# Optimization experiments

Hardware: AMD Instinct MI355X
Metric: run time of the kernel (lower is better)

## Reference

```python
import jax, jax.numpy as jnp
import numpy as np

N_NODES = 50000
N_EDGES = 640000
IN, HID, OUT = 128, 128, 64


def _sage_layer(x, src, dst, w_self, w_neigh, b):
    # DGL SAGEConv 'mean': fc_self(x) + fc_neigh(mean_{u in N(v)} x_u) + bias
    n = x.shape[0]
    deg = jax.ops.segment_sum(jnp.ones_like(src, dtype=x.dtype), dst, num_segments=n)
    neigh_sum = jax.ops.segment_sum(x[src], dst, num_segments=n)  # [N, F] irregular gather+reduce
    neigh = neigh_sum / jnp.maximum(deg, 1.0)[:, None]
    return x @ w_self + neigh @ w_neigh + b


def setup_inputs() -> dict:
    key = jax.random.key(0)
    ks = jax.random.split(key, 16)
    s = lambda fan_in: 1.0 / np.sqrt(fan_in)
    return {
        "x": jax.random.normal(ks[0], (N_NODES, IN), dtype=jnp.float32),
        "src": jax.random.randint(ks[1], (N_EDGES,), 0, N_NODES, dtype=jnp.int32),
        "dst": jax.random.randint(ks[2], (N_EDGES,), 0, N_NODES, dtype=jnp.int32),
        "w_self1": jax.random.normal(ks[3], (IN, HID), dtype=jnp.float32) * s(IN),
        "w_neigh1": jax.random.normal(ks[4], (IN, HID), dtype=jnp.float32) * s(IN),
        "b1": jnp.zeros((HID,), dtype=jnp.float32),
        "w_self2": jax.random.normal(ks[5], (HID, HID), dtype=jnp.float32) * s(HID),
        "w_neigh2": jax.random.normal(ks[6], (HID, HID), dtype=jnp.float32) * s(HID),
        "b2": jnp.zeros((HID,), dtype=jnp.float32),
        "w_self3": jax.random.normal(ks[7], (HID, OUT), dtype=jnp.float32) * s(HID),
        "w_neigh3": jax.random.normal(ks[8], (HID, OUT), dtype=jnp.float32) * s(HID),
        "b3": jnp.zeros((OUT,), dtype=jnp.float32),
    }


def reference(x, src, dst, w_self1, w_neigh1, b1, w_self2, w_neigh2, b2, w_self3, w_neigh3, b3):
    h = _sage_layer(x, src, dst, w_self1, w_neigh1, b1)
    h = jax.nn.relu(h)  # dropout omitted (eval mode)
    h = _sage_layer(h, src, dst, w_self2, w_neigh2, b2)
    h = jax.nn.relu(h)
    h = _sage_layer(h, src, dst, w_self3, w_neigh3, b3)
    return h
```

## Files before the change

kernel.cpp:

```cpp
#include <hip/hip_runtime.h>

static constexpr int F = 128;
static constexpr int MAXB = 32;

typedef __attribute__((ext_vector_type(8))) short bf16x8;
typedef __attribute__((ext_vector_type(4))) float f32x4;
typedef __attribute__((ext_vector_type(2))) float f32x2;

__device__ __forceinline__ unsigned short f2b(float f) {
    unsigned int u = __float_as_uint(f);
    u += 0x7fffu + ((u >> 16) & 1u);
    return (unsigned short)(u >> 16);
}
__device__ __forceinline__ float b2f(unsigned int s) {
    return __uint_as_float(s << 16);
}

#if __has_builtin(__builtin_elementwise_fma)
__device__ __forceinline__ f32x2 fma2(f32x2 a, f32x2 b, f32x2 c) { return __builtin_elementwise_fma(a, b, c); }
#else
__device__ __forceinline__ f32x2 fma2(f32x2 a, f32x2 b, f32x2 c) {
    f32x2 r; r[0] = fmaf(a[0], b[0], c[0]); r[1] = fmaf(a[1], b[1], c[1]); return r;
}
#endif

#if __has_builtin(__builtin_amdgcn_cvt_pk_f32_fp8) && __has_builtin(__builtin_amdgcn_cvt_pk_fp8_f32)
__device__ __forceinline__ f32x2 q2f_lo(unsigned int d) { return __builtin_amdgcn_cvt_pk_f32_fp8(d, false); }
__device__ __forceinline__ f32x2 q2f_hi(unsigned int d) { return __builtin_amdgcn_cvt_pk_f32_fp8(d, true);  }
__device__ __forceinline__ unsigned int f2q_pk4(float a, float b, float c, float d) {
    int p = __builtin_amdgcn_cvt_pk_fp8_f32(a, b, 0, false);
    p = __builtin_amdgcn_cvt_pk_fp8_f32(c, d, p, true);
    return (unsigned int)p;
}
__device__ __forceinline__ unsigned char f2q1(float v) {
    return (unsigned char)(__builtin_amdgcn_cvt_pk_fp8_f32(v, v, 0, false) & 0xff);
}
#else
__device__ __forceinline__ float q2f1(unsigned int b) {
    const unsigned s = b >> 7, e = (b >> 3) & 15, m = b & 7;
    float v = e ? __uint_as_float(((e - 7 + 127) << 23) | (m << 20))
                : (float)m * 0.001953125f;
    return s ? -v : v;
}
__device__ __forceinline__ f32x2 q2f_lo(unsigned int d) { f32x2 r; r[0] = q2f1(d & 0xff); r[1] = q2f1((d >> 8) & 0xff); return r; }
__device__ __forceinline__ f32x2 q2f_hi(unsigned int d) { f32x2 r; r[0] = q2f1((d >> 16) & 0xff); r[1] = q2f1((d >> 24) & 0xff); return r; }
__device__ __forceinline__ unsigned char f2q1(float f) {
    float cf = fminf(fmaxf(f, -448.f), 448.f);
    unsigned u = __float_as_uint(cf);
    unsigned s = (u >> 31) << 7;
    int e = (int)((u >> 23) & 255) - 127;
    unsigned m = u & 0x7fffff;
    if (e < -6) return (unsigned char)s;
    unsigned keep = m >> 20, rest = m & 0xfffff;
    keep += (rest > 0x80000u) || (rest == 0x80000u && (keep & 1));
    e += (int)(keep >> 3); keep &= 7;
    if (e > 8) { e = 8; keep = 6; }
    return (unsigned char)(s | ((unsigned)(e + 7) << 3) | keep);
}
__device__ __forceinline__ unsigned int f2q_pk4(float a, float b, float c, float d) {
    return (unsigned)f2q1(a) | ((unsigned)f2q1(b) << 8) | ((unsigned)f2q1(c) << 16) | ((unsigned)f2q1(d) << 24);
}
#endif

__global__ __launch_bounds__(256) void prep_kernel(const float* __restrict__ x,
                                                   unsigned short* __restrict__ xb,
                                                   unsigned int* __restrict__ xq, int n4,
                                                   int* __restrict__ cnt, int nNodes,
                                                   const float* __restrict__ ws1, const float* __restrict__ wn1,
                                                   const float* __restrict__ ws2, const float* __restrict__ wn2,
                                                   const float* __restrict__ ws3, const float* __restrict__ wn3,
                                                   unsigned short* __restrict__ wt1,
                                                   unsigned short* __restrict__ wt2,
                                                   unsigned short* __restrict__ wt3d) {
    const int id = blockIdx.x * 256 + threadIdx.x;
    if (id < n4) {
        const float4 v = reinterpret_cast<const float4*>(x)[id];
        uint2 o;
        o.x = (unsigned)f2b(v.x) | ((unsigned)f2b(v.y) << 16);
        o.y = (unsigned)f2b(v.z) | ((unsigned)f2b(v.w) << 16);
        reinterpret_cast<uint2*>(xb)[id] = o;
        xq[id] = f2q_pk4(v.x, v.y, v.z, v.w);
    }
    if (id < nNodes) cnt[id] = 0;
    if (id < 128 * 256) {
        const int k = id & 255, c = id >> 8;
        wt1[id] = f2b((k < 128) ? ws1[k * 128 + c] : wn1[(k - 128) * 128 + c]);
        wt2[id] = f2b((k < 128) ? ws2[k * 128 + c] : wn2[(k - 128) * 128 + c]);
    }
    if (id < 128 * 128) {
        const int k = id & 127, c = id >> 7;
        wt3d[id] = f2b((c < 64) ? ws3[k * 64 + c] : wn3[k * 64 + (c - 64)]);
    }
}

__global__ __launch_bounds__(256) void fill8_kernel(const int* __restrict__ src,
                                                    const int* __restrict__ dst,
                                                    int* __restrict__ cnt,
                                                    unsigned short* __restrict__ col2,
                                                    int nE, int npx) {
    const int part = blockIdx.x & 7;
    const int e = (blockIdx.x >> 3) * 256 + threadIdx.x;
    if (e >= nE) return;
    const int d = dst[e];
    if ((unsigned)(d - part * npx) < (unsigned)npx) {
        const int pos = atomicAdd(&cnt[d], 1);
        if (pos < MAXB) col2[(size_t)d * MAXB + pos] = (unsigned short)src[e];
    }
}

__global__ __launch_bounds__(256) void gather_q_kernel(const unsigned char* __restrict__ xq,
                                                       const int* __restrict__ cnt,
                                                       const unsigned short* __restrict__ col2,
                                                       unsigned short* __restrict__ nb, int nNodes) {
    const int grp  = (blockIdx.x * 256 + threadIdx.x) >> 3;
    const int lane = threadIdx.x & 7;
    if (grp >= nNodes) return;
    const int degr = cnt[grp];
    const int deg  = degr < MAXB ? degr : MAXB;
    const unsigned short* __restrict__ cp = col2 + (size_t)grp * MAXB;
    const int qb = lane << 4;

    f32x2 acc2[8];
#pragma unroll
    for (int k = 0; k < 8; ++k) acc2[k] = f32x2{0.f, 0.f};

    for (int j = 0; j < deg; j += 8) {
        const uint4 iv = *reinterpret_cast<const uint4*>(cp + j);
        const int idx[8] = { (int)(iv.x & 0xffffu), (int)(iv.x >> 16),
                             (int)(iv.y & 0xffffu), (int)(iv.y >> 16),
                             (int)(iv.z & 0xffffu), (int)(iv.z >> 16),
                             (int)(iv.w & 0xffffu), (int)(iv.w >> 16) };
        f32x2 wg2[8];
#pragma unroll
        for (int m = 0; m < 8; ++m) {
            const float w = (j + m < deg) ? 1.f : 0.f;
            wg2[m] = f32x2{w, w};
        }
        uint4 v[8];
#pragma unroll
        for (int m = 0; m < 8; ++m)
            v[m] = *reinterpret_cast<const uint4*>(xq + (size_t)idx[m] * F + qb);
#pragma unroll
        for (int m = 0; m < 8; ++m) {
            const unsigned int dw[4] = {v[m].x, v[m].y, v[m].z, v[m].w};
#pragma unroll
            for (int d = 0; d < 4; ++d) {
                acc2[2*d + 0] = fma2(q2f_lo(dw[d]), wg2[m], acc2[2*d + 0]);
                acc2[2*d + 1] = fma2(q2f_hi(dw[d]), wg2[m], acc2[2*d + 1]);
            }
        }
    }

    const float inv = 1.0f / (float)(degr > 1 ? degr : 1);
    uint4 o1, o2;
    o1.x = (unsigned)f2b(acc2[0][0] * inv) | ((unsigned)f2b(acc2[0][1] * inv) << 16);
    o1.y = (unsigned)f2b(acc2[1][0] * inv) | ((unsigned)f2b(acc2[1][1] * inv) << 16);
    o1.z = (unsigned)f2b(acc2[2][0] * inv) | ((unsigned)f2b(acc2[2][1] * inv) << 16);
    o1.w = (unsigned)f2b(acc2[3][0] * inv) | ((unsigned)f2b(acc2[3][1] * inv) << 16);
    o2.x = (unsigned)f2b(acc2[4][0] * inv) | ((unsigned)f2b(acc2[4][1] * inv) << 16);
    o2.y = (unsigned)f2b(acc2[5][0] * inv) | ((unsigned)f2b(acc2[5][1] * inv) << 16);
    o2.z = (unsigned)f2b(acc2[6][0] * inv) | ((unsigned)f2b(acc2[6][1] * inv) << 16);
    o2.w = (unsigned)f2b(acc2[7][0] * inv) | ((unsigned)f2b(acc2[7][1] * inv) << 16);
    unsigned short* op = nb + (size_t)grp * F + (lane << 4);
    *reinterpret_cast<uint4*>(op)     = o1;
    *reinterpret_cast<uint4*>(op + 8) = o2;
}

__global__ __launch_bounds__(256) void gather_f_kernel(const float* __restrict__ ys3,
                                                       const unsigned char* __restrict__ yn3q,
                                                       const int* __restrict__ cnt,
                                                       const unsigned short* __restrict__ col2,
                                                       float* __restrict__ out, int nNodes) {
    const int grp  = (blockIdx.x * 256 + threadIdx.x) >> 2;
    const int lane = threadIdx.x & 3;
    if (grp >= nNodes) return;
    const int degr = cnt[grp];
    const int deg  = degr < MAXB ? degr : MAXB;
    const unsigned short* __restrict__ cp = col2 + (size_t)grp * MAXB;
    const int qb = lane << 4;

    f32x2 acc2[8];
#pragma unroll
    for (int k = 0; k < 8; ++k) acc2[k] = f32x2{0.f, 0.f};

    for (int j = 0; j < deg; j += 8) {
        const uint4 iv = *reinterpret_cast<const uint4*>(cp + j);
        const int idx[8] = { (int)(iv.x & 0xffffu), (int)(iv.x >> 16),
                             (int)(iv.y & 0xffffu), (int)(iv.y >> 16),
                             (int)(iv.z & 0xffffu), (int)(iv.z >> 16),
                             (int)(iv.w & 0xffffu), (int)(iv.w >> 16) };
        f32x2 wg2[8];
#pragma unroll
        for (int m = 0; m < 8; ++m) {
            const float w = (j + m < deg) ? 1.f : 0.f;
            wg2[m] = f32x2{w, w};
        }
        uint4 v[8];
#pragma unroll
        for (int m = 0; m < 8; ++m)
            v[m] = *reinterpret_cast<const uint4*>(yn3q + (size_t)idx[m] * 64 + qb);
#pragma unroll
        for (int m = 0; m < 8; ++m) {
            const unsigned int dw[4] = {v[m].x, v[m].y, v[m].z, v[m].w};
#pragma unroll
            for (int d = 0; d < 4; ++d) {
                acc2[2*d + 0] = fma2(q2f_lo(dw[d]), wg2[m], acc2[2*d + 0]);
                acc2[2*d + 1] = fma2(q2f_hi(dw[d]), wg2[m], acc2[2*d + 1]);
            }
        }
    }

    const float inv = 1.0f / (float)(degr > 1 ? degr : 1);
    const float* sp = ys3 + (size_t)grp * 64 + (lane << 4);
    float*       op = out + (size_t)grp * 64 + (lane << 4);
#pragma unroll
    for (int d = 0; d < 4; ++d) {
        const float4 s = *reinterpret_cast<const float4*>(sp + d * 4);
        float4 o;
        o.x = s.x + acc2[2*d][0]     * inv;
        o.y = s.y + acc2[2*d][1]     * inv;
        o.z = s.z + acc2[2*d + 1][0] * inv;
        o.w = s.w + acc2[2*d + 1][1] * inv;
        *reinterpret_cast<float4*>(op + d * 4) = o;
    }
}

__global__ __launch_bounds__(256, 4) void mfma_layer1(const unsigned short* __restrict__ xb,
                                                      const unsigned short* __restrict__ nbuf,
                                                      const unsigned short* __restrict__ wt,
                                                      const float* __restrict__ bias,
                                                      unsigned short* __restrict__ outb,
                                                      unsigned char* __restrict__ outq, int nRows)
{
    __shared__ __align__(16) unsigned short Acat[64 * 256];

    const int tid  = threadIdx.x;
    const int row0 = blockIdx.x * 64;

    for (int i = tid; i < 2048; i += 256) {
        const int r  = i >> 5;
        const int ch = i & 31;
        const int g  = row0 + r;
        uint4 v = make_uint4(0u, 0u, 0u, 0u);
        if (g < nRows) {
            const unsigned short* s = (ch < 16) ? xb : nbuf;
            v = *reinterpret_cast<const uint4*>(s + (size_t)g * F + (ch & 15) * 8);
        }
        const int off = (ch * 16) ^ ((r & 7) << 4);
        *reinterpret_cast<uint4*>(reinterpret_cast<char*>(Acat) + r * 512 + off) = v;
    }
    __syncthreads();

    const int lane = tid & 63;
    const int w    = tid >> 6;
    const int lm   = lane & 15;
    const int lq   = lane >> 4;
    const int colBase = w * 32;

    f32x4 acc[4][2];
#pragma unroll
    for (int rt = 0; rt < 4; ++rt) {
        acc[rt][0] = f32x4{0.f, 0.f, 0.f, 0.f};
        acc[rt][1] = f32x4{0.f, 0.f, 0.f, 0.f};
    }

    const char* abase = reinterpret_cast<const char*>(Acat);
#pragma unroll
    for (int k0 = 0; k0 < 256; k0 += 32) {
        bf16x8 b[2];
#pragma unroll
        for (int c = 0; c < 2; ++c)
            b[c] = *reinterpret_cast<const bf16x8*>(
                wt + (size_t)(colBase + c * 16 + lm) * 256 + k0 + lq * 8);
#pragma unroll
        for (int rt = 0; rt < 4; ++rt) {
            const int arow = rt * 16 + lm;
            const int aoff = (k0 * 2 + lq * 16) ^ ((arow & 7) << 4);
            const bf16x8 a = *reinterpret_cast<const bf16x8*>(abase + arow * 512 + aoff);
#pragma unroll
            for (int c = 0; c < 2; ++c)
                acc[rt][c] = __builtin_amdgcn_mfma_f32_16x16x32_bf16(a, b[c], acc[rt][c], 0, 0, 0);
        }
    }

#pragma unroll
    for (int rt = 0; rt < 4; ++rt) {
#pragma unroll
        for (int c = 0; c < 2; ++c) {
            const int colIdx = colBase + c * 16 + lm;
            const float bv = bias[colIdx];
#pragma unroll
            for (int i = 0; i < 4; ++i) {
                const int grow = row0 + rt * 16 + lq * 4 + i;
                if (grow >= nRows) continue;
                const float v = fmaxf(acc[rt][c][i] + bv, 0.f);
                outb[(size_t)grow * F + colIdx] = f2b(v);
                outq[(size_t)grow * F + colIdx] = f2q1(v);
            }
        }
    }
}

__global__ __launch_bounds__(256, 4) void mfma_fused23(const unsigned short* __restrict__ h1b,
                                                       const unsigned short* __restrict__ nbuf,
                                                       const unsigned short* __restrict__ wt2,
                                                       const float* __restrict__ b2,
                                                       const unsigned short* __restrict__ wt3d,
                                                       const float* __restrict__ b3,
                                                       float* __restrict__ ys3,
                                                       unsigned char* __restrict__ yn3q, int nRows)
{
    __shared__ __align__(16) unsigned short Acat[64 * 256];

    const int tid  = threadIdx.x;
    const int row0 = blockIdx.x * 64;

    for (int i = tid; i < 2048; i += 256) {
        const int r  = i >> 5;
        const int ch = i & 31;
        const int g  = row0 + r;
        uint4 v = make_uint4(0u, 0u, 0u, 0u);
        if (g < nRows) {
            const unsigned short* s = (ch < 16) ? h1b : nbuf;
            v = *reinterpret_cast<const uint4*>(s + (size_t)g * F + (ch & 15) * 8);
        }
        const int off = (ch * 16) ^ ((r & 7) << 4);
        *reinterpret_cast<uint4*>(reinterpret_cast<char*>(Acat) + r * 512 + off) = v;
    }
    __syncthreads();

    const int lane = tid & 63;
    const int w    = tid >> 6;
    const int lm   = lane & 15;
    const int lq   = lane >> 4;
    const int colBase = w * 32;

    f32x4 acc[4][2];
#pragma unroll
    for (int rt = 0; rt < 4; ++rt) {
        acc[rt][0] = f32x4{0.f, 0.f, 0.f, 0.f};
        acc[rt][1] = f32x4{0.f, 0.f, 0.f, 0.f};
    }

    const char* abase = reinterpret_cast<const char*>(Acat);

#pragma unroll
    for (int k0 = 0; k0 < 256; k0 += 32) {
        bf16x8 b[2];
#pragma unroll
        for (int c = 0; c < 2; ++c)
            b[c] = *reinterpret_cast<const bf16x8*>(
                wt2 + (size_t)(colBase + c * 16 + lm) * 256 + k0 + lq * 8);
#pragma unroll
        for (int rt = 0; rt < 4; ++rt) {
            const int arow = rt * 16 + lm;
            const int aoff = (k0 * 2 + lq * 16) ^ ((arow & 7) << 4);
            const bf16x8 a = *reinterpret_cast<const bf16x8*>(abase + arow * 512 + aoff);
#pragma unroll
            for (int c = 0; c < 2; ++c)
                acc[rt][c] = __builtin_amdgcn_mfma_f32_16x16x32_bf16(a, b[c], acc[rt][c], 0, 0, 0);
        }
    }

    __syncthreads();

    {
        char* a2 = reinterpret_cast<char*>(Acat);
#pragma unroll
        for (int rt = 0; rt < 4; ++rt) {
#pragma unroll
            for (int c = 0; c < 2; ++c) {
                const int colIdx = colBase + c * 16 + lm;
                const float bv = b2[colIdx];
                const int chunkOff = (colIdx >> 3) << 4;
                const int inChunk  = (colIdx & 7) << 1;
#pragma unroll
                for (int i = 0; i < 4; ++i) {
                    const int r = rt * 16 + lq * 4 + i;
                    const float v = fmaxf(acc[rt][c][i] + bv, 0.f);
                    const int off = (chunkOff ^ ((r & 7) << 4)) + inChunk;
                    *reinterpret_cast<unsigned short*>(a2 + r * 256 + off) = f2b(v);
                }
            }
        }
    }
    __syncthreads();

#pragma unroll
    for (int rt = 0; rt < 4; ++rt) {
        acc[rt][0] = f32x4{0.f, 0.f, 0.f, 0.f};
        acc[rt][1] = f32x4{0.f, 0.f, 0.f, 0.f};
    }
#pragma unroll
    for (int k0 = 0; k0 < 128; k0 += 32) {
        bf16x8 b[2];
#pragma unroll
        for (int c = 0; c < 2; ++c)
            b[c] = *reinterpret_cast<const bf16x8*>(
                wt3d + (size_t)(colBase + c * 16 + lm) * 128 + k0 + lq * 8);
#pragma unroll
        for (int rt = 0; rt < 4; ++rt) {
            const int arow = rt * 16 + lm;
            const int aoff = (k0 * 2 + lq * 16) ^ ((arow & 7) << 4);
            const bf16x8 a = *reinterpret_cast<const bf16x8*>(abase + arow * 256 + aoff);
#pragma unroll
            for (int c = 0; c < 2; ++c)
                acc[rt][c] = __builtin_amdgcn_mfma_f32_16x16x32_bf16(a, b[c], acc[rt][c], 0, 0, 0);
        }
    }

#pragma unroll
    for (int rt = 0; rt < 4; ++rt) {
#pragma unroll
        for (int c = 0; c < 2; ++c) {
            const int colIdx = colBase + c * 16 + lm;
#pragma unroll
            for (int i = 0; i < 4; ++i) {
                const int grow = row0 + rt * 16 + lq * 4 + i;
                if (grow >= nRows) continue;
                if (colIdx < 64) {
                    ys3[(size_t)grow * 64 + colIdx] = acc[rt][c][i] + b3[colIdx];
                } else {
                    yn3q[(size_t)grow * 64 + (colIdx - 64)] = f2q1(acc[rt][c][i]);
                }
            }
        }
    }
}

extern "C" void kernel_launch(void* const* d_in, const int* in_sizes, int n_in,
                              void* d_out, int out_size, void* d_ws, size_t ws_size,
                              hipStream_t stream) {
    const float* x   = (const float*)d_in[0];
    const int*   src = (const int*)  d_in[1];
    const int*   dst = (const int*)  d_in[2];
    const float* ws1 = (const float*)d_in[3];
    const float* wn1 = (const float*)d_in[4];
    const float* b1  = (const float*)d_in[5];
    const float* ws2 = (const float*)d_in[6];
    const float* wn2 = (const float*)d_in[7];
    const float* b2  = (const float*)d_in[8];
    const float* ws3 = (const float*)d_in[9];
    const float* wn3 = (const float*)d_in[10];
    const float* b3  = (const float*)d_in[11];
    float* out = (float*)d_out;

    const int N = in_sizes[0] / F;
    const int E = in_sizes[1];
    const int n4 = N * F / 4;
    const int npx = (N + 7) / 8;

    char* w = (char*)d_ws;
    const size_t cntBytes  = ((size_t)N * 4 + 511) & ~(size_t)511;
    const size_t col2Bytes = ((size_t)N * MAXB * 2 + 511) & ~(size_t)511;
    int*            cnt  = (int*)(w);
    unsigned short* col2 = (unsigned short*)(w + cntBytes);
    unsigned short* xb   = (unsigned short*)(w + cntBytes + col2Bytes);
    unsigned short* nb   = xb  + (size_t)N * F;
    unsigned short* h1b  = nb  + (size_t)N * F;
    unsigned char*  xq   = (unsigned char*)(h1b + (size_t)N * F);
    unsigned char*  h1q  = xq  + (size_t)N * F;
    unsigned char*  yn3q = h1q + (size_t)N * F;
    float*          ys3  = (float*)(yn3q + (size_t)N * 64 + 256);
    unsigned short* wt1  = (unsigned short*)(ys3 + (size_t)N * 64);
    unsigned short* wt2  = wt1 + 128 * 256;
    unsigned short* wt3d = wt2 + 128 * 256;

    const dim3 blk(256);
    const int prepGrid = (n4 + 255) / 256;
    const int edgeGrid = (E + 255) / 256;
    const int gqGrid   = (int)(((size_t)N * 8 + 255) / 256);
    const int gfGrid   = (int)(((size_t)N * 4 + 255) / 256);
    const int mfmaGrid = (N + 63) / 64;

    prep_kernel<<<prepGrid, blk, 0, stream>>>(x, xb, (unsigned int*)xq, n4, cnt, N,
                                              ws1, wn1, ws2, wn2, ws3, wn3, wt1, wt2, wt3d);
    fill8_kernel<<<edgeGrid * 8, blk, 0, stream>>>(src, dst, cnt, col2, E, npx);

    gather_q_kernel<<<gqGrid, blk, 0, stream>>>(xq, cnt, col2, nb, N);
    mfma_layer1<<<mfmaGrid, blk, 0, stream>>>(xb, nb, wt1, b1, h1b, h1q, N);

    gather_q_kernel<<<gqGrid, blk, 0, stream>>>(h1q, cnt, col2, nb, N);
    mfma_fused23<<<mfmaGrid, blk, 0, stream>>>(h1b, nb, wt2, b2, wt3d, b3, ys3, yn3q, N);

    gather_f_kernel<<<gfGrid, blk, 0, stream>>>(ys3, yn3q, cnt, col2, out, N);
}
```

Before: 131.3 us.

## Fuse neighbor gather into MFMA layer kernels, dropping the intermediate buffer

The gather-mean of quantized neighbor features now runs inside the MFMA kernels: each block gathers the neighbor rows for its 64 nodes directly into the shared-memory A tile, next to the self features. This removes two separate gather launches and the write and re-read of the bf16 neighbor buffer in global memory. In exchange, each block runs a long irregular gather phase before its matrix multiply. Occupancy is bounded by the 32KB shared tile, so gather latency may be harder to hide than in the standalone high-occupancy gather kernel.

```diff
diff --git a/kernel.cpp b/kernel.cpp
--- a/kernel.cpp
+++ b/kernel.cpp
@@ -108,16 +108,13 @@
     }
 }
 
-__global__ __launch_bounds__(256) void gather_q_kernel(const unsigned char* __restrict__ xq,
-                                                       const int* __restrict__ cnt,
-                                                       const unsigned short* __restrict__ col2,
-                                                       unsigned short* __restrict__ nb, int nNodes) {
-    const int grp  = (blockIdx.x * 256 + threadIdx.x) >> 3;
-    const int lane = threadIdx.x & 7;
-    if (grp >= nNodes) return;
-    const int degr = cnt[grp];
+__device__ __forceinline__ void gather_node(const unsigned char* __restrict__ xq,
+                                            const int* __restrict__ cnt,
+                                            const unsigned short* __restrict__ col2,
+                                            int node, int lane, uint4& o1, uint4& o2) {
+    const int degr = cnt[node];
     const int deg  = degr < MAXB ? degr : MAXB;
-    const unsigned short* __restrict__ cp = col2 + (size_t)grp * MAXB;
+    const unsigned short* __restrict__ cp = col2 + (size_t)node * MAXB;
     const int qb = lane << 4;
 
     f32x2 acc2[8];
@@ -152,7 +149,6 @@
     }
 
     const float inv = 1.0f / (float)(degr > 1 ? degr : 1);
-    uint4 o1, o2;
     o1.x = (unsigned)f2b(acc2[0][0] * inv) | ((unsigned)f2b(acc2[0][1] * inv) << 16);
     o1.y = (unsigned)f2b(acc2[1][0] * inv) | ((unsigned)f2b(acc2[1][1] * inv) << 16);
     o1.z = (unsigned)f2b(acc2[2][0] * inv) | ((unsigned)f2b(acc2[2][1] * inv) << 16);
@@ -161,9 +157,222 @@
     o2.y = (unsigned)f2b(acc2[5][0] * inv) | ((unsigned)f2b(acc2[5][1] * inv) << 16);
     o2.z = (unsigned)f2b(acc2[6][0] * inv) | ((unsigned)f2b(acc2[6][1] * inv) << 16);
     o2.w = (unsigned)f2b(acc2[7][0] * inv) | ((unsigned)f2b(acc2[7][1] * inv) << 16);
-    unsigned short* op = nb + (size_t)grp * F + (lane << 4);
-    *reinterpret_cast<uint4*>(op)     = o1;
-    *reinterpret_cast<uint4*>(op + 8) = o2;
+}
+
+__device__ __forceinline__ void build_Atile(unsigned short* __restrict__ Acat,
+                                            const unsigned short* __restrict__ selfb,
+                                            const unsigned char* __restrict__ gq,
+                                            const int* __restrict__ cnt,
+                                            const unsigned short* __restrict__ col2,
+                                            int nRows, int row0, int tid) {
+    {
+        const int g    = tid >> 3;
+        const int lane = tid & 7;
+        for (int rr = g; rr < 64; rr += 32) {
+            const int node = row0 + rr;
+            uint4 o1 = make_uint4(0u,0u,0u,0u), o2 = make_uint4(0u,0u,0u,0u);
+            if (node < nRows) gather_node(gq, cnt, col2, node, lane, o1, o2);
+            char* base = reinterpret_cast<char*>(Acat) + rr * 512;
+            const int c0 = 16 + lane * 2;
+            *reinterpret_cast<uint4*>(base + ((c0 * 16)       ^ ((rr & 7) << 4))) = o1;
+            *reinterpret_cast<uint4*>(base + (((c0 + 1) * 16) ^ ((rr & 7) << 4))) = o2;
+        }
+    }
+    for (int i = tid; i < 1024; i += 256) {
+        const int r  = i >> 4;
+        const int ch = i & 15;
+        const int g  = row0 + r;
+        uint4 v = make_uint4(0u, 0u, 0u, 0u);
+        if (g < nRows)
+            v = *reinterpret_cast<const uint4*>(selfb + (size_t)g * F + ch * 8);
+        const int off = (ch * 16) ^ ((r & 7) << 4);
+        *reinterpret_cast<uint4*>(reinterpret_cast<char*>(Acat) + r * 512 + off) = v;
+    }
+}
+
+__global__ __launch_bounds__(256, 4) void mfma_g1(const unsigned char* __restrict__ xq,
+                                                  const unsigned short* __restrict__ xb,
+                                                  const int* __restrict__ cnt,
+                                                  const unsigned short* __restrict__ col2,
+                                                  const unsigned short* __restrict__ wt,
+                                                  const float* __restrict__ bias,
+                                                  unsigned short* __restrict__ outb,
+                                                  unsigned char* __restrict__ outq, int nRows)
+{
+    __shared__ __align__(16) unsigned short Acat[64 * 256];
+
+    const int tid  = threadIdx.x;
+    const int row0 = blockIdx.x * 64;
+
+    build_Atile(Acat, xb, xq, cnt, col2, nRows, row0, tid);
+    __syncthreads();
+
+    const int lane = tid & 63;
+    const int w    = tid >> 6;
+    const int lm   = lane & 15;
+    const int lq   = lane >> 4;
+    const int colBase = w * 32;
+
+    f32x4 acc[4][2];
+#pragma unroll
+    for (int rt = 0; rt < 4; ++rt) {
+        acc[rt][0] = f32x4{0.f, 0.f, 0.f, 0.f};
+        acc[rt][1] = f32x4{0.f, 0.f, 0.f, 0.f};
+    }
+
+    const char* abase = reinterpret_cast<const char*>(Acat);
+#pragma unroll
+    for (int k0 = 0; k0 < 256; k0 += 32) {
+        bf16x8 b[2];
+#pragma unroll
+        for (int c = 0; c < 2; ++c)
+            b[c] = *reinterpret_cast<const bf16x8*>(
+                wt + (size_t)(colBase + c * 16 + lm) * 256 + k0 + lq * 8);
+#pragma unroll
+        for (int rt = 0; rt < 4; ++rt) {
+            const int arow = rt * 16 + lm;
+            const int aoff = (k0 * 2 + lq * 16) ^ ((arow & 7) << 4);
+            const bf16x8 a = *reinterpret_cast<const bf16x8*>(abase + arow * 512 + aoff);
+#pragma unroll
+            for (int c = 0; c < 2; ++c)
+                acc[rt][c] = __builtin_amdgcn_mfma_f32_16x16x32_bf16(a, b[c], acc[rt][c], 0, 0, 0);
+        }
+    }
+
+#pragma unroll
+    for (int rt = 0; rt < 4; ++rt) {
+#pragma unroll
+        for (int c = 0; c < 2; ++c) {
+            const int colIdx = colBase + c * 16 + lm;
+            const float bv = bias[colIdx];
+#pragma unroll
+            for (int i = 0; i < 4; ++i) {
+                const int grow = row0 + rt * 16 + lq * 4 + i;
+                if (grow >= nRows) continue;
+                const float v = fmaxf(acc[rt][c][i] + bv, 0.f);
+                outb[(size_t)grow * F + colIdx] = f2b(v);
+                outq[(size_t)grow * F + colIdx] = f2q1(v);
+            }
+        }
+    }
+}
+
+__global__ __launch_bounds__(256, 4) void mfma_g23(const unsigned char* __restrict__ h1q,
+                                                   const unsigned short* __restrict__ h1b,
+                                                   const int* __restrict__ cnt,
+                                                   const unsigned short* __restrict__ col2,
+                                                   const unsigned short* __restrict__ wt2,
+                                                   const float* __restrict__ b2,
+                                                   const unsigned short* __restrict__ wt3d,
+                                                   const float* __restrict__ b3,
+                                                   float* __restrict__ ys3,
+                                                   unsigned char* __restrict__ yn3q, int nRows)
+{
+    __shared__ __align__(16) unsigned short Acat[64 * 256];
+
+    const int tid  = threadIdx.x;
+    const int row0 = blockIdx.x * 64;
+
+    build_Atile(Acat, h1b, h1q, cnt, col2, nRows, row0, tid);
+    __syncthreads();
+
+    const int lane = tid & 63;
+    const int w    = tid >> 6;
+    const int lm   = lane & 15;
+    const int lq   = lane >> 4;
+    const int colBase = w * 32;
+
+    f32x4 acc[4][2];
+#pragma unroll
+    for (int rt = 0; rt < 4; ++rt) {
+        acc[rt][0] = f32x4{0.f, 0.f, 0.f, 0.f};
+        acc[rt][1] = f32x4{0.f, 0.f, 0.f, 0.f};
+    }
+
+    const char* abase = reinterpret_cast<const char*>(Acat);
+
+#pragma unroll
+    for (int k0 = 0; k0 < 256; k0 += 32) {
+        bf16x8 b[2];
+#pragma unroll
+        for (int c = 0; c < 2; ++c)
+            b[c] = *reinterpret_cast<const bf16x8*>(
+                wt2 + (size_t)(colBase + c * 16 + lm) * 256 + k0 + lq * 8);
+#pragma unroll
+        for (int rt = 0; rt < 4; ++rt) {
+            const int arow = rt * 16 + lm;
+            const int aoff = (k0 * 2 + lq * 16) ^ ((arow & 7) << 4);
+            const bf16x8 a = *reinterpret_cast<const bf16x8*>(abase + arow * 512 + aoff);
+#pragma unroll
+            for (int c = 0; c < 2; ++c)
+                acc[rt][c] = __builtin_amdgcn_mfma_f32_16x16x32_bf16(a, b[c], acc[rt][c], 0, 0, 0);
+        }
+    }
+
+    __syncthreads();
+
+    {
+        char* a2 = reinterpret_cast<char*>(Acat);
+#pragma unroll
+        for (int rt = 0; rt < 4; ++rt) {
+#pragma unroll
+            for (int c = 0; c < 2; ++c) {
+                const int colIdx = colBase + c * 16 + lm;
+                const float bv = b2[colIdx];
+                const int chunkOff = (colIdx >> 3) << 4;
+                const int inChunk  = (colIdx & 7) << 1;
+#pragma unroll
+                for (int i = 0; i < 4; ++i) {
+                    const int r = rt * 16 + lq * 4 + i;
+                    const float v = fmaxf(acc[rt][c][i] + bv, 0.f);
+                    const int off = (chunkOff ^ ((r & 7) << 4)) + inChunk;
+                    *reinterpret_cast<unsigned short*>(a2 + r * 256 + off) = f2b(v);
+                }
+            }
+        }
+    }
+    __syncthreads();
+
+#pragma unroll
+    for (int rt = 0; rt < 4; ++rt) {
+        acc[rt][0] = f32x4{0.f, 0.f, 0.f, 0.f};
+        acc[rt][1] = f32x4{0.f, 0.f, 0.f, 0.f};
+    }
+#pragma unroll
+    for (int k0 = 0; k0 < 128; k0 += 32) {
+        bf16x8 b[2];
+#pragma unroll
+        for (int c = 0; c < 2; ++c)
+            b[c] = *reinterpret_cast<const bf16x8*>(
+                wt3d + (size_t)(colBase + c * 16 + lm) * 128 + k0 + lq * 8);
+#pragma unroll
+        for (int rt = 0; rt < 4; ++rt) {
+            const int arow = rt * 16 + lm;
+            const int aoff = (k0 * 2 + lq * 16) ^ ((arow & 7) << 4);
+            const bf16x8 a = *reinterpret_cast<const bf16x8*>(abase + arow * 256 + aoff);
+#pragma unroll
+            for (int c = 0; c < 2; ++c)
+                acc[rt][c] = __builtin_amdgcn_mfma_f32_16x16x32_bf16(a, b[c], acc[rt][c], 0, 0, 0);
+        }
+    }
+
+#pragma unroll
+    for (int rt = 0; rt < 4; ++rt) {
+#pragma unroll
+        for (int c = 0; c < 2; ++c) {
+            const int colIdx = colBase + c * 16 + lm;
+#pragma unroll
+            for (int i = 0; i < 4; ++i) {
+                const int grow = row0 + rt * 16 + lq * 4 + i;
+                if (grow >= nRows) continue;
+                if (colIdx < 64) {
+                    ys3[(size_t)grow * 64 + colIdx] = acc[rt][c][i] + b3[colIdx];
+                } else {
+                    yn3q[(size_t)grow * 64 + (colIdx - 64)] = f2q1(acc[rt][c][i]);
+                }
+            }
+        }
+    }
 }
 
 __global__ __launch_bounds__(256) void gather_f_kernel(const float* __restrict__ ys3,
@@ -222,209 +431,6 @@
         o.z = s.z + acc2[2*d + 1][0] * inv;
         o.w = s.w + acc2[2*d + 1][1] * inv;
         *reinterpret_cast<float4*>(op + d * 4) = o;
-    }
-}
-
-__global__ __launch_bounds__(256, 4) void mfma_layer1(const unsigned short* __restrict__ xb,
-                                                      const unsigned short* __restrict__ nbuf,
-                                                      const unsigned short* __restrict__ wt,
-                                                      const float* __restrict__ bias,
-                                                      unsigned short* __restrict__ outb,
-                                                      unsigned char* __restrict__ outq, int nRows)
-{
-    __shared__ __align__(16) unsigned short Acat[64 * 256];
-
-    const int tid  = threadIdx.x;
-    const int row0 = blockIdx.x * 64;
-
-    for (int i = tid; i < 2048; i += 256) {
-        const int r  = i >> 5;
-        const int ch = i & 31;
-        const int g  = row0 + r;
-        uint4 v = make_uint4(0u, 0u, 0u, 0u);
-        if (g < nRows) {
-            const unsigned short* s = (ch < 16) ? xb : nbuf;
-            v = *reinterpret_cast<const uint4*>(s + (size_t)g * F + (ch & 15) * 8);
-        }
-        const int off = (ch * 16) ^ ((r & 7) << 4);
-        *reinterpret_cast<uint4*>(reinterpret_cast<char*>(Acat) + r * 512 + off) = v;
-    }
-    __syncthreads();
-
-    const int lane = tid & 63;
-    const int w    = tid >> 6;
-    const int lm   = lane & 15;
-    const int lq   = lane >> 4;
-    const int colBase = w * 32;
-
-    f32x4 acc[4][2];
-#pragma unroll
-    for (int rt = 0; rt < 4; ++rt) {
-        acc[rt][0] = f32x4{0.f, 0.f, 0.f, 0.f};
-        acc[rt][1] = f32x4{0.f, 0.f, 0.f, 0.f};
-    }
-
-    const char* abase = reinterpret_cast<const char*>(Acat);
-#pragma unroll
-    for (int k0 = 0; k0 < 256; k0 += 32) {
-        bf16x8 b[2];
-#pragma unroll
-        for (int c = 0; c < 2; ++c)
-            b[c] = *reinterpret_cast<const bf16x8*>(
-                wt + (size_t)(colBase + c * 16 + lm) * 256 + k0 + lq * 8);
-#pragma unroll
-        for (int rt = 0; rt < 4; ++rt) {
-            const int arow = rt * 16 + lm;
-            const int aoff = (k0 * 2 + lq * 16) ^ ((arow & 7) << 4);
-            const bf16x8 a = *reinterpret_cast<const bf16x8*>(abase + arow * 512 + aoff);
-#pragma unroll
-            for (int c = 0; c < 2; ++c)
-                acc[rt][c] = __builtin_amdgcn_mfma_f32_16x16x32_bf16(a, b[c], acc[rt][c], 0, 0, 0);
-        }
-    }
-
-#pragma unroll
-    for (int rt = 0; rt < 4; ++rt) {
-#pragma unroll
-        for (int c = 0; c < 2; ++c) {
-            const int colIdx = colBase + c * 16 + lm;
-            const float bv = bias[colIdx];
-#pragma unroll
-            for (int i = 0; i < 4; ++i) {
-                const int grow = row0 + rt * 16 + lq * 4 + i;
-                if (grow >= nRows) continue;
-                const float v = fmaxf(acc[rt][c][i] + bv, 0.f);
-                outb[(size_t)grow * F + colIdx] = f2b(v);
-                outq[(size_t)grow * F + colIdx] = f2q1(v);
-            }
-        }
-    }
-}
-
-__global__ __launch_bounds__(256, 4) void mfma_fused23(const unsigned short* __restrict__ h1b,
-                                                       const unsigned short* __restrict__ nbuf,
-                                                       const unsigned short* __restrict__ wt2,
-                                                       const float* __restrict__ b2,
-                                                       const unsigned short* __restrict__ wt3d,
-                                                       const float* __restrict__ b3,
-                                                       float* __restrict__ ys3,
-                                                       unsigned char* __restrict__ yn3q, int nRows)
-{
-    __shared__ __align__(16) unsigned short Acat[64 * 256];
-
-    const int tid  = threadIdx.x;
-    const int row0 = blockIdx.x * 64;
-
-    for (int i = tid; i < 2048; i += 256) {
-        const int r  = i >> 5;
-        const int ch = i & 31;
-        const int g  = row0 + r;
-        uint4 v = make_uint4(0u, 0u, 0u, 0u);
-        if (g < nRows) {
-            const unsigned short* s = (ch < 16) ? h1b : nbuf;
-            v = *reinterpret_cast<const uint4*>(s + (size_t)g * F + (ch & 15) * 8);
-        }
-        const int off = (ch * 16) ^ ((r & 7) << 4);
-        *reinterpret_cast<uint4*>(reinterpret_cast<char*>(Acat) + r * 512 + off) = v;
-    }
-    __syncthreads();
-
-    const int lane = tid & 63;
-    const int w    = tid >> 6;
-    const int lm   = lane & 15;
-    const int lq   = lane >> 4;
-    const int colBase = w * 32;
-
-    f32x4 acc[4][2];
-#pragma unroll
-    for (int rt = 0; rt < 4; ++rt) {
-        acc[rt][0] = f32x4{0.f, 0.f, 0.f, 0.f};
-        acc[rt][1] = f32x4{0.f, 0.f, 0.f, 0.f};
-    }
-
-    const char* abase = reinterpret_cast<const char*>(Acat);
-
-#pragma unroll
-    for (int k0 = 0; k0 < 256; k0 += 32) {
-        bf16x8 b[2];
-#pragma unroll
-        for (int c = 0; c < 2; ++c)
-            b[c] = *reinterpret_cast<const bf16x8*>(
-                wt2 + (size_t)(colBase + c * 16 + lm) * 256 + k0 + lq * 8);
-#pragma unroll
-        for (int rt = 0; rt < 4; ++rt) {
-            const int arow = rt * 16 + lm;
-            const int aoff = (k0 * 2 + lq * 16) ^ ((arow & 7) << 4);
-            const bf16x8 a = *reinterpret_cast<const bf16x8*>(abase + arow * 512 + aoff);
-#pragma unroll
-            for (int c = 0; c < 2; ++c)
-                acc[rt][c] = __builtin_amdgcn_mfma_f32_16x16x32_bf16(a, b[c], acc[rt][c], 0, 0, 0);
-        }
-    }
-
-    __syncthreads();
-
-    {
-        char* a2 = reinterpret_cast<char*>(Acat);
-#pragma unroll
-        for (int rt = 0; rt < 4; ++rt) {
-#pragma unroll
-            for (int c = 0; c < 2; ++c) {
-                const int colIdx = colBase + c * 16 + lm;
-                const float bv = b2[colIdx];
-                const int chunkOff = (colIdx >> 3) << 4;
-                const int inChunk  = (colIdx & 7) << 1;
-#pragma unroll
-                for (int i = 0; i < 4; ++i) {
-                    const int r = rt * 16 + lq * 4 + i;
-                    const float v = fmaxf(acc[rt][c][i] + bv, 0.f);
-                    const int off = (chunkOff ^ ((r & 7) << 4)) + inChunk;
-                    *reinterpret_cast<unsigned short*>(a2 + r * 256 + off) = f2b(v);
-                }
-            }
-        }
-    }
-    __syncthreads();
-
-#pragma unroll
-    for (int rt = 0; rt < 4; ++rt) {
-        acc[rt][0] = f32x4{0.f, 0.f, 0.f, 0.f};
-        acc[rt][1] = f32x4{0.f, 0.f, 0.f, 0.f};
-    }
-#pragma unroll
-    for (int k0 = 0; k0 < 128; k0 += 32) {
-        bf16x8 b[2];
-#pragma unroll
-        for (int c = 0; c < 2; ++c)
-            b[c] = *reinterpret_cast<const bf16x8*>(
-                wt3d + (size_t)(colBase + c * 16 + lm) * 128 + k0 + lq * 8);
-#pragma unroll
-        for (int rt = 0; rt < 4; ++rt) {
-            const int arow = rt * 16 + lm;
-            const int aoff = (k0 * 2 + lq * 16) ^ ((arow & 7) << 4);
-            const bf16x8 a = *reinterpret_cast<const bf16x8*>(abase + arow * 256 + aoff);
-#pragma unroll
-            for (int c = 0; c < 2; ++c)
-                acc[rt][c] = __builtin_amdgcn_mfma_f32_16x16x32_bf16(a, b[c], acc[rt][c], 0, 0, 0);
-        }
-    }
-
-#pragma unroll
-    for (int rt = 0; rt < 4; ++rt) {
-#pragma unroll
-        for (int c = 0; c < 2; ++c) {
-            const int colIdx = colBase + c * 16 + lm;
-#pragma unroll
-            for (int i = 0; i < 4; ++i) {
-                const int grow = row0 + rt * 16 + lq * 4 + i;
-                if (grow >= nRows) continue;
-                if (colIdx < 64) {
-                    ys3[(size_t)grow * 64 + colIdx] = acc[rt][c][i] + b3[colIdx];
-                } else {
-                    yn3q[(size_t)grow * 64 + (colIdx - 64)] = f2q1(acc[rt][c][i]);
-                }
-            }
-        }
     }
 }
 
@@ -456,8 +462,7 @@
     int*            cnt  = (int*)(w);
     unsigned short* col2 = (unsigned short*)(w + cntBytes);
     unsigned short* xb   = (unsigned short*)(w + cntBytes + col2Bytes);
-    unsigned short* nb   = xb  + (size_t)N * F;
-    unsigned short* h1b  = nb  + (size_t)N * F;
+    unsigned short* h1b  = xb  + (size_t)N * F;
     unsigned char*  xq   = (unsigned char*)(h1b + (size_t)N * F);
     unsigned char*  h1q  = xq  + (size_t)N * F;
     unsigned char*  yn3q = h1q + (size_t)N * F;
@@ -469,7 +474,6 @@
     const dim3 blk(256);
     const int prepGrid = (n4 + 255) / 256;
     const int edgeGrid = (E + 255) / 256;
-    const int gqGrid   = (int)(((size_t)N * 8 + 255) / 256);
     const int gfGrid   = (int)(((size_t)N * 4 + 255) / 256);
     const int mfmaGrid = (N + 63) / 64;
 
@@ -477,11 +481,8 @@
                                               ws1, wn1, ws2, wn2, ws3, wn3, wt1, wt2, wt3d);
     fill8_kernel<<<edgeGrid * 8, blk, 0, stream>>>(src, dst, cnt, col2, E, npx);
 
-    gather_q_kernel<<<gqGrid, blk, 0, stream>>>(xq, cnt, col2, nb, N);
-    mfma_layer1<<<mfmaGrid, blk, 0, stream>>>(xb, nb, wt1, b1, h1b, h1q, N);
-
-    gather_q_kernel<<<gqGrid, blk, 0, stream>>>(h1q, cnt, col2, nb, N);
-    mfma_fused23<<<mfmaGrid, blk, 0, stream>>>(h1b, nb, wt2, b2, wt3d, b3, ys3, yn3q, N);
+    mfma_g1<<<mfmaGrid, blk, 0, stream>>>(xq, xb, cnt, col2, wt1, b1, h1b, h1q, N);
+    mfma_g23<<<mfmaGrid, blk, 0, stream>>>(h1q, h1b, cnt, col2, wt2, b2, wt3d, b3, ys3, yn3q, N);
 
     gather_f_kernel<<<gfGrid, blk, 0, stream>>>(ys3, yn3q, cnt, col2, out, N);
 }
```

New measurement: 117.2 us. -10.7%, faster.
